# Kernel optimization log

Hardware: AMD Instinct MI355X
Metric: run time of the kernel (lower is better)

Reference implementation:

```python
import jax, jax.numpy as jnp
import numpy as np

B, N, DIM, H, DH = 2, 256, 512, 8, 64
CLAMP = 40.0


def rmsnorm(x, w):
    eps = jnp.finfo(x.dtype).eps
    return x * jax.lax.rsqrt(jnp.mean(x * x, axis=-1, keepdims=True) + eps) * w


def strassen_attend(q, k1, k2, v1, v2, sim_clamp_value):
    # q,k1,k2: [b,h,n,d]; v1,v2: [b,h,n,dv]
    scale = q.shape[-1] ** -0.5
    q = q * scale
    sim1 = jnp.einsum('bhid,bhjd->bhij', q, k1)            # q . k1
    sim2 = jnp.einsum('bhid,bhkd->bhik', q, k2)            # q . k2
    sim3 = jnp.einsum('bhjd,bhkd->bhjk', k1, k2) * scale   # k1 . k2
    c = sim_clamp_value
    e1 = jnp.exp(jnp.clip(sim1, -c, c))
    e2 = jnp.exp(jnp.clip(sim2, -c, c))
    e3 = jnp.exp(jnp.clip(sim3, -c, c))
    # joint softmax over (j,k) of sim1[i,j]+sim2[i,k]+sim3[j,k], values v1[j]*v2[k]
    # factorized via exp(a+b+c)=exp(a)exp(b)exp(c):
    # D[b,h,i,j,d] = sum_k e2[i,k] e3[j,k] v2[k,d]
    D = jnp.einsum('bhik,bhjk,bhkd->bhijd', e2, e3, v2)
    num = jnp.einsum('bhij,bhjd,bhijd->bhid', e1, v1, D)
    den_ij = jnp.einsum('bhik,bhjk->bhij', e2, e3)
    den = jnp.einsum('bhij,bhij->bhi', e1, den_ij)
    return num / den[..., None]


def setup_inputs() -> dict:
    key = jax.random.key(0)
    k0, k1, k2 = jax.random.split(key, 3)
    x = jax.random.normal(k0, (B, N, DIM), dtype=jnp.float32)
    w_qkv = jax.random.normal(k1, (DIM, 5 * H * DH), dtype=jnp.float32) * (DIM ** -0.5)
    w_out = jax.random.normal(k2, (H * DH, DIM), dtype=jnp.float32) * ((H * DH) ** -0.5)
    q_norm_w = jnp.ones((DH,), jnp.float32)
    k1_norm_w = jnp.ones((DH,), jnp.float32)
    k2_norm_w = jnp.ones((DH,), jnp.float32)
    return {'x': x, 'w_qkv': w_qkv, 'w_out': w_out,
            'q_norm_w': q_norm_w, 'k1_norm_w': k1_norm_w, 'k2_norm_w': k2_norm_w}


def reference(x, w_qkv, w_out, q_norm_w, k1_norm_w, k2_norm_w):
    qkv = x @ w_qkv                                         # [b,n,5*h*d]
    q, k1, k2, v1, v2 = jnp.split(qkv, np.cumsum([H * DH] * 4), axis=-1)
    split_heads = lambda t: t.reshape(B, N, H, DH).transpose(0, 2, 1, 3)
    q, k1, k2, v1, v2 = map(split_heads, (q, k1, k2, v1, v2))
    q = rmsnorm(q, q_norm_w)
    k1 = rmsnorm(k1, k1_norm_w)
    k2 = rmsnorm(k2, k2_norm_w)
    out = strassen_attend(q, k1, k2, v1, v2, CLAMP)         # [b,h,n,d]
    out = out.transpose(0, 2, 1, 3).reshape(B, N, H * DH)
    return out @ w_out
```

## Files before the change

kernel.cpp:

```cpp
#include <hip/hip_runtime.h>
#include <hip/hip_bf16.h>


namespace {
constexpr int kN = 256, kH = 8, kDH = 64;
constexpr int kBH = 16;
constexpr int kBN = 512;
constexpr int kDIM = 512;
constexpr int kQKV = 2560;
constexpr float kEps = 1.1920928955078125e-07f;

typedef unsigned short u16;
typedef __attribute__((ext_vector_type(8))) short short8v;
typedef __attribute__((ext_vector_type(4))) float float4v;

constexpr size_t OF_XB   = 0;
constexpr size_t OF_WT   = OF_XB   + 131072;
constexpr size_t OF_WOT  = OF_WT   + 655360;
constexpr size_t OF_QKVB = OF_WOT  + 131072;
constexpr size_t OF_QB   = OF_QKVB + 655360;
constexpr size_t OF_K1B  = OF_QB   + 131072;
constexpr size_t OF_K2B  = OF_K1B  + 131072;
constexpr size_t OF_V1   = OF_K2B  + 131072;
constexpr size_t OF_V2   = OF_V1   + 262144;
constexpr size_t OF_E1F  = OF_V2   + 262144;
constexpr size_t OF_E2B  = OF_E1F  + 1048576;
constexpr size_t OF_E3B  = OF_E2B  + 524288;
constexpr size_t OF_NUM  = OF_E3B  + 524288;
constexpr size_t OF_DEN  = OF_NUM  + 262144;
constexpr size_t OF_ATNB = OF_DEN  + 4096;
}

__device__ __forceinline__ unsigned int bf16_rne(float a) {
  unsigned int u = __float_as_uint(a);
  return (u + 0x7fffu + ((u >> 16) & 1u)) >> 16;
}
__device__ __forceinline__ unsigned int pk2_bf16(float a, float b) {
  unsigned int ua = bf16_rne(a);
  unsigned int ub = __float_as_uint(b);
  ub = (ub + 0x7fffu + ((ub >> 16) & 1u)) & 0xffff0000u;
  return ua | ub;
}
__device__ __forceinline__ float bf2f(u16 v) {
  return __uint_as_float(((unsigned)v) << 16);
}

__global__ __launch_bounds__(256)
void conv_bf16(const float* __restrict__ in, u16* __restrict__ out) {
  const int id = blockIdx.x * 256 + threadIdx.x;
  float4 v = ((const float4*)in)[id];
  ushort4 o;
  o.x = (u16)bf16_rne(v.x); o.y = (u16)bf16_rne(v.y);
  o.z = (u16)bf16_rne(v.z); o.w = (u16)bf16_rne(v.w);
  ((ushort4*)out)[id] = o;
}

__global__ __launch_bounds__(256)
void transpose_bf16(const float* __restrict__ in, u16* __restrict__ out,
                    int rows, int cols) {
  __shared__ float tile[32][33];
  const int tx = threadIdx.x & 31, ty8 = threadIdx.x >> 5;
  const int c0 = blockIdx.x * 32, r0 = blockIdx.y * 32;
#pragma unroll
  for (int rr = 0; rr < 4; ++rr) {
    int r = ty8 + rr * 8;
    tile[r][tx] = in[(size_t)(r0 + r) * cols + c0 + tx];
  }
  __syncthreads();
#pragma unroll
  for (int rr = 0; rr < 4; ++rr) {
    int r = ty8 + rr * 8;
    out[(size_t)(c0 + r) * rows + r0 + tx] = (u16)bf16_rne(tile[tx][r]);
  }
}

template <bool F32OUT>
__global__ __launch_bounds__(256)
void gemm_mfma(const u16* __restrict__ A, const u16* __restrict__ BT,
               void* __restrict__ C, int M, int N, int K) {
  const int t = threadIdx.x, lane = t & 63, w = t >> 6;
  const int lrow = lane & 15, lk = lane >> 4;
  const int m0 = blockIdx.y * 64 + w * 16;
  const int n0 = blockIdx.x * 64;
  float4v acc[4] = {};
#pragma unroll 4
  for (int kk = 0; kk < K; kk += 32) {
    short8v aF = *(const short8v*)(A + (size_t)(m0 + lrow) * K + kk + lk * 8);
#pragma unroll
    for (int n = 0; n < 4; ++n) {
      short8v bF = *(const short8v*)(BT + (size_t)(n0 + n * 16 + lrow) * K + kk + lk * 8);
      acc[n] = __builtin_amdgcn_mfma_f32_16x16x32_bf16(aF, bF, acc[n], 0, 0, 0);
    }
  }
#pragma unroll
  for (int n = 0; n < 4; ++n)
#pragma unroll
    for (int r = 0; r < 4; ++r) {
      const int row = m0 + lk * 4 + r, col = n0 + n * 16 + lrow;
      if (F32OUT) ((float*)C)[(size_t)row * N + col] = acc[n][r];
      else        ((u16*)C)[(size_t)row * N + col] = (u16)bf16_rne(acc[n][r]);
    }
}

__global__ __launch_bounds__(64)
void rms_layout(const u16* __restrict__ qkvb,
                const float* __restrict__ wq, const float* __restrict__ wk1,
                const float* __restrict__ wk2,
                u16* __restrict__ Qb, u16* __restrict__ K1b,
                u16* __restrict__ K2b, float* __restrict__ V1,
                float* __restrict__ V2) {
  const int bnh = blockIdx.x;
  const int h = bnh & 7;
  const int bn = bnh >> 3;
  const int b = bn >> 8;
  const int d = threadIdx.x;
  const u16* row = qkvb + (size_t)bn * kQKV;
  const int base = h * 64 + d;
  float q  = bf2f(row[0 * 512 + base]);
  float k1 = bf2f(row[1 * 512 + base]);
  float k2 = bf2f(row[2 * 512 + base]);
  float v1 = bf2f(row[3 * 512 + base]);
  float v2 = bf2f(row[4 * 512 + base]);
  float sq = q * q, s1 = k1 * k1, s2 = k2 * k2;
#pragma unroll
  for (int m = 32; m >= 1; m >>= 1) {
    sq += __shfl_xor(sq, m);
    s1 += __shfl_xor(s1, m);
    s2 += __shfl_xor(s2, m);
  }
  const float rq = rsqrtf(sq * (1.0f / 64) + kEps);
  const float r1 = rsqrtf(s1 * (1.0f / 64) + kEps);
  const float r2 = rsqrtf(s2 * (1.0f / 64) + kEps);
  const int bh = b * kH + h;
  const int n = bn & 255;
  const size_t o = ((size_t)bh * kN + n) * kDH + d;
  Qb[o]  = (u16)bf16_rne(q * rq * wq[d]);
  K1b[o] = (u16)bf16_rne(k1 * r1 * wk1[d]);
  K2b[o] = (u16)bf16_rne(k2 * r2 * wk2[d]);
  V1[o] = v1;
  V2[o] = v2;
}

__global__ __launch_bounds__(256)
void sims_mfma(const u16* __restrict__ Qb, const u16* __restrict__ K1b,
               const u16* __restrict__ K2b, float* __restrict__ E1f,
               u16* __restrict__ E2b, u16* __restrict__ E3b) {
  const int bh = blockIdx.x, type = blockIdx.y;
  const int it = blockIdx.z >> 2, jt = blockIdx.z & 3;
  const int t = threadIdx.x, lane = t & 63, w = t >> 6;
  const int lrow = lane & 15, lk = lane >> 4;
  const u16* Ap = (type == 2 ? K1b : Qb) + (size_t)bh * 16384;
  const u16* Bp = (type == 0 ? K1b : K2b) + (size_t)bh * 16384;
  const int i0 = it * 64 + w * 16, j0 = jt * 64;
  float4v acc[4] = {};
#pragma unroll
  for (int kk = 0; kk < 2; ++kk) {
    short8v aF = *(const short8v*)(Ap + (size_t)(i0 + lrow) * 64 + kk * 32 + lk * 8);
#pragma unroll
    for (int n = 0; n < 4; ++n) {
      short8v bF = *(const short8v*)(Bp + (size_t)(j0 + n * 16 + lrow) * 64 + kk * 32 + lk * 8);
      acc[n] = __builtin_amdgcn_mfma_f32_16x16x32_bf16(aF, bF, acc[n], 0, 0, 0);
    }
  }
  if (type == 0) {
    float* Ep = E1f + (size_t)bh * 65536;
#pragma unroll
    for (int n = 0; n < 4; ++n)
#pragma unroll
      for (int r = 0; r < 4; ++r) {
        float s = acc[n][r] * 0.125f;
        s = fminf(fmaxf(s, -40.0f), 40.0f);
        Ep[(size_t)(i0 + lk * 4 + r) * 256 + j0 + n * 16 + lrow] = __expf(s);
      }
  } else {
    u16* Ep = (type == 1 ? E2b : E3b) + (size_t)bh * 65536;
#pragma unroll
    for (int n = 0; n < 4; ++n)
#pragma unroll
      for (int r = 0; r < 4; ++r) {
        float s = acc[n][r] * 0.125f;
        s = fminf(fmaxf(s, -40.0f), 40.0f);
        Ep[(size_t)(i0 + lk * 4 + r) * 256 + j0 + n * 16 + lrow] =
            (u16)bf16_rne(__expf(s));
      }
  }
}

__global__ __launch_bounds__(256)
void strassen_v2(const u16* __restrict__ E2b, const float* __restrict__ E1f,
                 const u16* __restrict__ E3b, const float* __restrict__ V1,
                 const float* __restrict__ V2, float* __restrict__ NUM,
                 float* __restrict__ DEN) {
  __shared__ __align__(16) u16 Bp[2048 * 8];
  __shared__ float v2T[4][256];

  const int dblk = blockIdx.x;
  const int iblk = blockIdx.y;
  const int bh = blockIdx.z;
  const bool isden = (dblk == 16);
  const int d0 = dblk * 4;
  const int t = threadIdx.x;
  const int lane = t & 63, w = t >> 6;
  const int lrow = lane & 15, lk = lane >> 4;

  const size_t ebase = (size_t)bh * 65536;
  const u16* e2p = E2b + ebase;
  const float* e1p = E1f + ebase;
  const u16* e3p = E3b + ebase;

#pragma unroll
  for (int r = 0; r < 4; ++r) {
    const int i2 = t + 256 * r;
    const int dd = i2 >> 8, k = i2 & 255;
    v2T[dd][k] = isden ? 1.0f : V2[((size_t)bh * kN + k) * kDH + d0 + dd];
  }

  float p[4][4] = {};
  const int irowA = iblk * 64 + w * 16 + lrow;
  const int irowD = iblk * 64 + w * 16 + lk * 4;

  for (int ks = 0; ks < 4; ++ks) {
    const int k0 = ks * 64;
    __syncthreads();
#pragma unroll
    for (int s = 0; s < 8; ++s) {
      const int slot = t + 256 * s;
      const int ln = slot & 63, sub = (slot >> 6) & 1;
      const int n = (slot >> 7) & 3, jj = slot >> 9;
      const int jrow = jj * 64 + n * 16 + (ln & 15);
      const int kcol = k0 + sub * 32 + (ln >> 4) * 8;
      *(uint4*)(Bp + (size_t)slot * 8) =
          *(const uint4*)(e3p + (size_t)jrow * 256 + kcol);
    }
    __syncthreads();
    short8v aFd[4][2];
#pragma unroll
    for (int sub = 0; sub < 2; ++sub) {
      const int kseg = k0 + sub * 32 + lk * 8;
      const short8v araw = *(const short8v*)(e2p + (size_t)irowA * 256 + kseg);
      float af[8];
#pragma unroll
      for (int e = 0; e < 8; ++e) af[e] = bf2f((u16)araw[e]);
#pragma unroll
      for (int dd = 0; dd < 4; ++dd) {
        const float* vp = &v2T[dd][kseg];
        union { short8v s; uint4 u; } pk;
        pk.u.x = pk2_bf16(af[0] * vp[0], af[1] * vp[1]);
        pk.u.y = pk2_bf16(af[2] * vp[2], af[3] * vp[3]);
        pk.u.z = pk2_bf16(af[4] * vp[4], af[5] * vp[5]);
        pk.u.w = pk2_bf16(af[6] * vp[6], af[7] * vp[7]);
        aFd[dd][sub] = pk.s;
      }
    }
#pragma unroll 1
    for (int jt = 0; jt < 4; ++jt) {
#pragma unroll
      for (int n = 0; n < 4; ++n) {
        float4v acc4[4] = {};
#pragma unroll
        for (int sub = 0; sub < 2; ++sub) {
          const short8v bF = *(const short8v*)(
              Bp + ((size_t)(((jt * 4 + n) * 2 + sub) * 64 + lane)) * 8);
#pragma unroll
          for (int dd = 0; dd < 4; ++dd)
            acc4[dd] = __builtin_amdgcn_mfma_f32_16x16x32_bf16(
                aFd[dd][sub], bF, acc4[dd], 0, 0, 0);
        }
        const int j = jt * 64 + n * 16 + lrow;
        float e1f[4];
#pragma unroll
        for (int r = 0; r < 4; ++r)
          e1f[r] = e1p[(size_t)(irowD + r) * 256 + j];
        float v1s[4];
        if (isden) {
          v1s[0] = v1s[1] = v1s[2] = v1s[3] = 1.0f;
        } else {
          const float4 v4 = *(const float4*)(V1 + ((size_t)bh * kN + j) * kDH + d0);
          v1s[0] = v4.x; v1s[1] = v4.y; v1s[2] = v4.z; v1s[3] = v4.w;
        }
#pragma unroll
        for (int dd = 0; dd < 4; ++dd)
#pragma unroll
          for (int r = 0; r < 4; ++r)
            p[dd][r] = fmaf(e1f[r] * v1s[dd], acc4[dd][r], p[dd][r]);
      }
    }
  }

#pragma unroll
  for (int dd = 0; dd < 4; ++dd)
#pragma unroll
    for (int r = 0; r < 4; ++r) {
      float v = p[dd][r];
      v += __shfl_xor(v, 1);
      v += __shfl_xor(v, 2);
      v += __shfl_xor(v, 4);
      v += __shfl_xor(v, 8);
      p[dd][r] = v;
    }
  if (lrow == 0) {
    if (!isden) {
#pragma unroll
      for (int r = 0; r < 4; ++r)
#pragma unroll
        for (int dd = 0; dd < 4; ++dd)
          NUM[((size_t)bh * kN + irowD + r) * kDH + d0 + dd] = p[dd][r];
    } else {
#pragma unroll
      for (int r = 0; r < 4; ++r)
        DEN[(size_t)bh * kN + irowD + r] = p[0][r];
    }
  }
}

__global__ __launch_bounds__(256)
void normalize_attn(const float* __restrict__ NUMp, const float* __restrict__ DENp,
                    u16* __restrict__ attnb) {
  const int idx = blockIdx.x * 256 + threadIdx.x;
  const int d = idx & 63;
  const int i = (idx >> 6) & 255;
  const int bh = idx >> 14;
  const int b = bh >> 3, h = bh & 7;
  const float v = NUMp[idx] / DENp[bh * kN + i];
  attnb[((size_t)(b * kN + i)) * kDIM + h * kDH + d] = (u16)bf16_rne(v);
}

extern "C" void kernel_launch(void* const* d_in, const int* in_sizes, int n_in,
                              void* d_out, int out_size, void* d_ws, size_t ws_size,
                              hipStream_t stream) {
  const float* x     = (const float*)d_in[0];
  const float* w_qkv = (const float*)d_in[1];
  const float* w_out = (const float*)d_in[2];
  const float* qw    = (const float*)d_in[3];
  const float* k1w   = (const float*)d_in[4];
  const float* k2w   = (const float*)d_in[5];

  float* ws = (float*)d_ws;
  u16* xb   = (u16*)(ws + OF_XB);
  u16* wT   = (u16*)(ws + OF_WT);
  u16* woT  = (u16*)(ws + OF_WOT);
  u16* qkvb = (u16*)(ws + OF_QKVB);
  u16* Qb   = (u16*)(ws + OF_QB);
  u16* K1b  = (u16*)(ws + OF_K1B);
  u16* K2b  = (u16*)(ws + OF_K2B);
  float* V1 = ws + OF_V1;
  float* V2 = ws + OF_V2;
  float* E1f = ws + OF_E1F;
  u16* E2b  = (u16*)(ws + OF_E2B);
  u16* E3b  = (u16*)(ws + OF_E3B);
  float* NUMp = ws + OF_NUM;
  float* DENp = ws + OF_DEN;
  u16* atnb = (u16*)(ws + OF_ATNB);

  conv_bf16<<<dim3(kBN * kDIM / 1024), 256, 0, stream>>>(x, xb);
  transpose_bf16<<<dim3(kQKV / 32, kDIM / 32), 256, 0, stream>>>(
      w_qkv, wT, kDIM, kQKV);
  transpose_bf16<<<dim3(kDIM / 32, kDIM / 32), 256, 0, stream>>>(
      w_out, woT, kDIM, kDIM);

  gemm_mfma<false><<<dim3(kQKV / 64, kBN / 64), 256, 0, stream>>>(
      xb, wT, qkvb, kBN, kQKV, kDIM);

  rms_layout<<<dim3(kBN * kH), 64, 0, stream>>>(
      qkvb, qw, k1w, k2w, Qb, K1b, K2b, V1, V2);

  sims_mfma<<<dim3(kBH, 3, 16), 256, 0, stream>>>(Qb, K1b, K2b, E1f, E2b, E3b);

  strassen_v2<<<dim3(17, 4, kBH), 256, 0, stream>>>(
      E2b, E1f, E3b, V1, V2, NUMp, DENp);

  normalize_attn<<<dim3(1024), 256, 0, stream>>>(NUMp, DENp, atnb);

  gemm_mfma<true><<<dim3(kDIM / 64, kBN / 64), 256, 0, stream>>>(
      atnb, woT, d_out, kBN, kDIM, kDIM);
}
```

Before: 224.3 us.

## Prepack E3 into MFMA fragment order and drop LDS staging in strassen kernel

The sims kernel now writes E3 straight into the MFMA B-fragment order through an LDS transpose, and writes E1 transposed so the strassen kernel can read it with float4 loads. V2 is stored transposed so its slices load as contiguous float4s. The strassen kernel no longer stages E3 or V2 in shared memory and has no __syncthreads. It is templated into separate numerator and denominator launches, so the denominator pass skips the V2 multiply and runs a single MFMA chain. This removes per-block LDS copies and barriers, but E3 fragments are now read from global/L2 by every block and the V2T write in rms_layout is strided.

```diff
diff --git a/kernel.cpp b/kernel.cpp
--- a/kernel.cpp
+++ b/kernel.cpp
@@ -22,11 +22,11 @@
 constexpr size_t OF_K1B  = OF_QB   + 131072;
 constexpr size_t OF_K2B  = OF_K1B  + 131072;
 constexpr size_t OF_V1   = OF_K2B  + 131072;
-constexpr size_t OF_V2   = OF_V1   + 262144;
-constexpr size_t OF_E1F  = OF_V2   + 262144;
-constexpr size_t OF_E2B  = OF_E1F  + 1048576;
-constexpr size_t OF_E3B  = OF_E2B  + 524288;
-constexpr size_t OF_NUM  = OF_E3B  + 524288;
+constexpr size_t OF_V2T  = OF_V1   + 262144;
+constexpr size_t OF_E1T  = OF_V2T  + 262144;
+constexpr size_t OF_E2B  = OF_E1T  + 1048576;
+constexpr size_t OF_E3F  = OF_E2B  + 524288;
+constexpr size_t OF_NUM  = OF_E3F  + 524288;
 constexpr size_t OF_DEN  = OF_NUM  + 262144;
 constexpr size_t OF_ATNB = OF_DEN  + 4096;
 }
@@ -108,7 +108,7 @@
                 const float* __restrict__ wk2,
                 u16* __restrict__ Qb, u16* __restrict__ K1b,
                 u16* __restrict__ K2b, float* __restrict__ V1,
-                float* __restrict__ V2) {
+                float* __restrict__ V2T) {
   const int bnh = blockIdx.x;
   const int h = bnh & 7;
   const int bn = bnh >> 3;
@@ -138,13 +138,14 @@
   K1b[o] = (u16)bf16_rne(k1 * r1 * wk1[d]);
   K2b[o] = (u16)bf16_rne(k2 * r2 * wk2[d]);
   V1[o] = v1;
-  V2[o] = v2;
+  V2T[((size_t)bh * kDH + d) * kN + n] = v2;
 }
 
 __global__ __launch_bounds__(256)
 void sims_mfma(const u16* __restrict__ Qb, const u16* __restrict__ K1b,
-               const u16* __restrict__ K2b, float* __restrict__ E1f,
-               u16* __restrict__ E2b, u16* __restrict__ E3b) {
+               const u16* __restrict__ K2b, float* __restrict__ E1T,
+               u16* __restrict__ E2b, u16* __restrict__ E3f) {
+  __shared__ __align__(16) u16 Lt[64 * 80];
   const int bh = blockIdx.x, type = blockIdx.y;
   const int it = blockIdx.z >> 2, jt = blockIdx.z & 3;
   const int t = threadIdx.x, lane = t & 63, w = t >> 6;
@@ -163,17 +164,17 @@
     }
   }
   if (type == 0) {
-    float* Ep = E1f + (size_t)bh * 65536;
+    float* Ep = E1T + (size_t)bh * 65536;
 #pragma unroll
     for (int n = 0; n < 4; ++n)
 #pragma unroll
       for (int r = 0; r < 4; ++r) {
         float s = acc[n][r] * 0.125f;
         s = fminf(fmaxf(s, -40.0f), 40.0f);
-        Ep[(size_t)(i0 + lk * 4 + r) * 256 + j0 + n * 16 + lrow] = __expf(s);
-      }
-  } else {
-    u16* Ep = (type == 1 ? E2b : E3b) + (size_t)bh * 65536;
+        Ep[(size_t)(j0 + n * 16 + lrow) * 256 + i0 + lk * 4 + r] = __expf(s);
+      }
+  } else if (type == 1) {
+    u16* Ep = E2b + (size_t)bh * 65536;
 #pragma unroll
     for (int n = 0; n < 4; ++n)
 #pragma unroll
@@ -183,21 +184,39 @@
         Ep[(size_t)(i0 + lk * 4 + r) * 256 + j0 + n * 16 + lrow] =
             (u16)bf16_rne(__expf(s));
       }
-  }
-}
-
-__global__ __launch_bounds__(256)
-void strassen_v2(const u16* __restrict__ E2b, const float* __restrict__ E1f,
-                 const u16* __restrict__ E3b, const float* __restrict__ V1,
-                 const float* __restrict__ V2, float* __restrict__ NUM,
+  } else {
+#pragma unroll
+    for (int n = 0; n < 4; ++n)
+#pragma unroll
+      for (int r = 0; r < 4; ++r) {
+        float s = acc[n][r] * 0.125f;
+        s = fminf(fmaxf(s, -40.0f), 40.0f);
+        Lt[(w * 16 + lk * 4 + r) * 80 + n * 16 + lrow] = (u16)bf16_rne(__expf(s));
+      }
+    __syncthreads();
+    u16* Ep = E3f + (size_t)bh * 65536;
+#pragma unroll
+    for (int ss = 0; ss < 2; ++ss) {
+      const int sl = ss * 256 + t;
+      const int nn = sl >> 7, sub = (sl >> 6) & 1, ln = sl & 63;
+      const int lr = ln & 15, lq = ln >> 4;
+      const uint4 v = *(const uint4*)&Lt[(nn * 16 + lr) * 80 + sub * 32 + lq * 8];
+      const size_t gslot = (size_t)((((it * 4 + nn) * 4 + jt) * 2 + sub) * 64 + ln);
+      *(uint4*)(Ep + gslot * 8) = v;
+    }
+  }
+}
+
+template <bool ISDEN>
+__global__ __launch_bounds__(256)
+void strassen_v3(const u16* __restrict__ E2b, const float* __restrict__ E1T,
+                 const u16* __restrict__ E3f, const float* __restrict__ V1,
+                 const float* __restrict__ V2T, float* __restrict__ NUM,
                  float* __restrict__ DEN) {
-  __shared__ __align__(16) u16 Bp[2048 * 8];
-  __shared__ float v2T[4][256];
-
+  constexpr int NDD = ISDEN ? 1 : 4;
   const int dblk = blockIdx.x;
   const int iblk = blockIdx.y;
   const int bh = blockIdx.z;
-  const bool isden = (dblk == 16);
   const int d0 = dblk * 4;
   const int t = threadIdx.x;
   const int lane = t & 63, w = t >> 6;
@@ -205,90 +224,77 @@
 
   const size_t ebase = (size_t)bh * 65536;
   const u16* e2p = E2b + ebase;
-  const float* e1p = E1f + ebase;
-  const u16* e3p = E3b + ebase;
-
-#pragma unroll
-  for (int r = 0; r < 4; ++r) {
-    const int i2 = t + 256 * r;
-    const int dd = i2 >> 8, k = i2 & 255;
-    v2T[dd][k] = isden ? 1.0f : V2[((size_t)bh * kN + k) * kDH + d0 + dd];
-  }
-
-  float p[4][4] = {};
+  const float* e1p = E1T + ebase;
+  const u16* e3p = E3f + ebase;
+  const float* v2p = V2T + ((size_t)bh * kDH + d0) * kN;
+
   const int irowA = iblk * 64 + w * 16 + lrow;
   const int irowD = iblk * 64 + w * 16 + lk * 4;
 
+  float p[NDD][4] = {};
+
+#pragma unroll 1
   for (int ks = 0; ks < 4; ++ks) {
-    const int k0 = ks * 64;
-    __syncthreads();
-#pragma unroll
-    for (int s = 0; s < 8; ++s) {
-      const int slot = t + 256 * s;
-      const int ln = slot & 63, sub = (slot >> 6) & 1;
-      const int n = (slot >> 7) & 3, jj = slot >> 9;
-      const int jrow = jj * 64 + n * 16 + (ln & 15);
-      const int kcol = k0 + sub * 32 + (ln >> 4) * 8;
-      *(uint4*)(Bp + (size_t)slot * 8) =
-          *(const uint4*)(e3p + (size_t)jrow * 256 + kcol);
-    }
-    __syncthreads();
-    short8v aFd[4][2];
+    short8v aFd[NDD][2];
 #pragma unroll
     for (int sub = 0; sub < 2; ++sub) {
-      const int kseg = k0 + sub * 32 + lk * 8;
+      const int kseg = ks * 64 + sub * 32 + lk * 8;
       const short8v araw = *(const short8v*)(e2p + (size_t)irowA * 256 + kseg);
-      float af[8];
-#pragma unroll
-      for (int e = 0; e < 8; ++e) af[e] = bf2f((u16)araw[e]);
-#pragma unroll
-      for (int dd = 0; dd < 4; ++dd) {
-        const float* vp = &v2T[dd][kseg];
-        union { short8v s; uint4 u; } pk;
-        pk.u.x = pk2_bf16(af[0] * vp[0], af[1] * vp[1]);
-        pk.u.y = pk2_bf16(af[2] * vp[2], af[3] * vp[3]);
-        pk.u.z = pk2_bf16(af[4] * vp[4], af[5] * vp[5]);
-        pk.u.w = pk2_bf16(af[6] * vp[6], af[7] * vp[7]);
-        aFd[dd][sub] = pk.s;
-      }
-    }
-#pragma unroll 1
+      if (ISDEN) {
+        aFd[0][sub] = araw;
+      } else {
+        float af[8];
+#pragma unroll
+        for (int e = 0; e < 8; ++e) af[e] = bf2f((u16)araw[e]);
+#pragma unroll
+        for (int dd = 0; dd < NDD; ++dd) {
+          const float4 va = *(const float4*)(v2p + (size_t)dd * kN + kseg);
+          const float4 vb = *(const float4*)(v2p + (size_t)dd * kN + kseg + 4);
+          union { short8v s; uint4 u; } pk;
+          pk.u.x = pk2_bf16(af[0] * va.x, af[1] * va.y);
+          pk.u.y = pk2_bf16(af[2] * va.z, af[3] * va.w);
+          pk.u.z = pk2_bf16(af[4] * vb.x, af[5] * vb.y);
+          pk.u.w = pk2_bf16(af[6] * vb.z, af[7] * vb.w);
+          aFd[dd][sub] = pk.s;
+        }
+      }
+    }
+#pragma unroll 2
     for (int jt = 0; jt < 4; ++jt) {
 #pragma unroll
       for (int n = 0; n < 4; ++n) {
-        float4v acc4[4] = {};
+        float4v acc4[NDD] = {};
 #pragma unroll
         for (int sub = 0; sub < 2; ++sub) {
           const short8v bF = *(const short8v*)(
-              Bp + ((size_t)(((jt * 4 + n) * 2 + sub) * 64 + lane)) * 8);
-#pragma unroll
-          for (int dd = 0; dd < 4; ++dd)
+              e3p + ((size_t)((((jt * 4 + n) * 4 + ks) * 2 + sub) * 64 + lane)) * 8);
+#pragma unroll
+          for (int dd = 0; dd < NDD; ++dd)
             acc4[dd] = __builtin_amdgcn_mfma_f32_16x16x32_bf16(
                 aFd[dd][sub], bF, acc4[dd], 0, 0, 0);
         }
         const int j = jt * 64 + n * 16 + lrow;
-        float e1f[4];
-#pragma unroll
-        for (int r = 0; r < 4; ++r)
-          e1f[r] = e1p[(size_t)(irowD + r) * 256 + j];
-        float v1s[4];
-        if (isden) {
-          v1s[0] = v1s[1] = v1s[2] = v1s[3] = 1.0f;
+        const float4 e4 = *(const float4*)(e1p + (size_t)j * 256 + irowD);
+        const float e1f[4] = {e4.x, e4.y, e4.z, e4.w};
+        if (ISDEN) {
+#pragma unroll
+          for (int r = 0; r < 4; ++r)
+            p[0][r] = fmaf(e1f[r], acc4[0][r], p[0][r]);
         } else {
           const float4 v4 = *(const float4*)(V1 + ((size_t)bh * kN + j) * kDH + d0);
-          v1s[0] = v4.x; v1s[1] = v4.y; v1s[2] = v4.z; v1s[3] = v4.w;
+          const float v1s[4] = {v4.x, v4.y, v4.z, v4.w};
+#pragma unroll
+          for (int dd = 0; dd < NDD; ++dd)
+#pragma unroll
+            for (int r = 0; r < 4; ++r)
+              p[dd][r] = fmaf(e1f[r] * v1s[dd], acc4[dd][r], p[dd][r]);
         }
-#pragma unroll
-        for (int dd = 0; dd < 4; ++dd)
-#pragma unroll
-          for (int r = 0; r < 4; ++r)
-            p[dd][r] = fmaf(e1f[r] * v1s[dd], acc4[dd][r], p[dd][r]);
-      }
-    }
-  }
-
-#pragma unroll
-  for (int dd = 0; dd < 4; ++dd)
+      }
+    }
+  }
+
+#pragma unroll
+  for (int dd = 0; dd < NDD; ++dd)
 #pragma unroll
     for (int r = 0; r < 4; ++r) {
       float v = p[dd][r];
@@ -299,11 +305,11 @@
       p[dd][r] = v;
     }
   if (lrow == 0) {
-    if (!isden) {
+    if (!ISDEN) {
 #pragma unroll
       for (int r = 0; r < 4; ++r)
 #pragma unroll
-        for (int dd = 0; dd < 4; ++dd)
+        for (int dd = 0; dd < NDD; ++dd)
           NUM[((size_t)bh * kN + irowD + r) * kDH + d0 + dd] = p[dd][r];
     } else {
 #pragma unroll
@@ -344,10 +350,10 @@
   u16* K1b  = (u16*)(ws + OF_K1B);
   u16* K2b  = (u16*)(ws + OF_K2B);
   float* V1 = ws + OF_V1;
-  float* V2 = ws + OF_V2;
-  float* E1f = ws + OF_E1F;
+  float* V2T = ws + OF_V2T;
+  float* E1T = ws + OF_E1T;
   u16* E2b  = (u16*)(ws + OF_E2B);
-  u16* E3b  = (u16*)(ws + OF_E3B);
+  u16* E3f  = (u16*)(ws + OF_E3F);
   float* NUMp = ws + OF_NUM;
   float* DENp = ws + OF_DEN;
   u16* atnb = (u16*)(ws + OF_ATNB);
@@ -362,12 +368,14 @@
       xb, wT, qkvb, kBN, kQKV, kDIM);
 
   rms_layout<<<dim3(kBN * kH), 64, 0, stream>>>(
-      qkvb, qw, k1w, k2w, Qb, K1b, K2b, V1, V2);
-
-  sims_mfma<<<dim3(kBH, 3, 16), 256, 0, stream>>>(Qb, K1b, K2b, E1f, E2b, E3b);
-
-  strassen_v2<<<dim3(17, 4, kBH), 256, 0, stream>>>(
-      E2b, E1f, E3b, V1, V2, NUMp, DENp);
+      qkvb, qw, k1w, k2w, Qb, K1b, K2b, V1, V2T);
+
+  sims_mfma<<<dim3(kBH, 3, 16), 256, 0, stream>>>(Qb, K1b, K2b, E1T, E2b, E3f);
+
+  strassen_v3<false><<<dim3(16, 4, kBH), 256, 0, stream>>>(
+      E2b, E1T, E3f, V1, V2T, NUMp, DENp);
+  strassen_v3<true><<<dim3(1, 4, kBH), 256, 0, stream>>>(
+      E2b, E1T, E3f, V1, V2T, NUMp, DENp);
 
   normalize_attn<<<dim3(1024), 256, 0, stream>>>(NUMp, DENp, atnb);
 
```

After: 245.7 us. 9.5% more time.
